# Performance work log

Measured on AMD Instinct MI355X. Metric: run time of the kernel, lower is better.

Reference implementation:

```python
import jax, jax.numpy as jnp
import numpy as np

NUM_HEADS = 16
HEAD_DIM = 32  # dim=512 / num_heads=16


def _rel_pos_bias(table, index, window_area):
    # table: [(2W-1)^2, H], index: [N, N] int -> bias [1, H, N, N]
    bias = table[index.reshape(-1)].reshape(window_area, window_area, -1)
    return jnp.transpose(bias, (2, 0, 1))[None]


def setup_inputs() -> dict:
    key = jax.random.key(0)
    ks = jax.random.split(key, 6)
    B, N, C = 256, 196, 512
    x = jax.random.normal(ks[0], (B, N, C), dtype=jnp.float32)
    qkv_w = jax.random.normal(ks[1], (3 * C, C), dtype=jnp.float32) * 0.02
    proj_w = jax.random.normal(ks[2], (C, C), dtype=jnp.float32) * 0.02
    proj_b = jax.random.normal(ks[3], (C,), dtype=jnp.float32) * 0.02
    rel_pos_bias_table = jax.random.normal(ks[4], (729, NUM_HEADS), dtype=jnp.float32) * 0.02
    rel_pos_index = jax.random.randint(ks[5], (N, N), 0, 729, dtype=jnp.int64)
    return {
        "x": x,
        "qkv_w": qkv_w,
        "proj_w": proj_w,
        "proj_b": proj_b,
        "rel_pos_bias_table": rel_pos_bias_table,
        "rel_pos_index": rel_pos_index,
        "window_area": N,
    }


def reference(x, qkv_w, proj_w, proj_b, rel_pos_bias_table, rel_pos_index, window_area):
    B, N, C = x.shape
    H, hd = NUM_HEADS, HEAD_DIM
    scale = hd ** -0.5
    # qkv projection (no bias), split into q,k,v: [B, H, N, hd]
    qkv = (x @ qkv_w.T).reshape(B, N, 3, H, hd)
    qkv = jnp.transpose(qkv, (2, 0, 3, 1, 4))
    q, k, v = qkv[0], qkv[1], qkv[2]
    attn = jnp.einsum("bhnd,bhmd->bhnm", q * scale, k)
    attn = attn + _rel_pos_bias(rel_pos_bias_table, rel_pos_index, window_area)
    attn = jax.nn.softmax(attn, axis=-1)
    out = jnp.einsum("bhnm,bhmd->bhnd", attn, v)
    out = jnp.transpose(out, (0, 2, 1, 3)).reshape(B, N, C)
    return out @ proj_w.T + proj_b
```

## Files before the change

kernel.cpp:

```cpp
#include <hip/hip_runtime.h>
#include <hip/hip_bf16.h>


typedef unsigned short u16;
typedef unsigned int u32;
typedef __attribute__((ext_vector_type(8))) short bf16x8;
typedef __attribute__((ext_vector_type(4))) float f32x4;

__device__ __forceinline__ u16 f2bf(float f) {
  union { float f; unsigned u; } c; c.f = f;
  unsigned r = ((c.u >> 16) & 1u) + 0x7fffu;
  return (u16)((c.u + r) >> 16);
}

__global__ __launch_bounds__(256) void cvt_f32_bf16(const float* __restrict__ in,
                                                    u16* __restrict__ out, int n) {
  int i = (blockIdx.x * 256 + threadIdx.x) * 4;
  if (i >= n) return;
  float4 v = *(const float4*)(in + i);
  ushort4 o;
  o.x = f2bf(v.x); o.y = f2bf(v.y); o.z = f2bf(v.z); o.w = f2bf(v.w);
  *(ushort4*)(out + i) = o;
}

__global__ __launch_bounds__(256) void zero_vt_pad(u16* __restrict__ vt) {
  int i = blockIdx.x * 256 + threadIdx.x;
  if (i >= 4096 * 32 * 36) return;
  int row = i / 36, c = i - row * 36;
  vt[row * 232 + 196 + c] = 0;
}

__global__ __launch_bounds__(256) void build_bias(const float* __restrict__ table,
                                                  const int* __restrict__ idx,
                                                  float* __restrict__ outb) {
  int e = blockIdx.x * 256 + threadIdx.x;
  int r = e & 3, lane = (e >> 2) & 63, rest = e >> 8;
  int mt = rest % 14; rest /= 14;
  int nt = rest % 13; int h = rest / 13;
  int n = nt * 16 + (lane & 15);
  int m = mt * 16 + ((lane >> 4) << 2) + r;
  float v;
  if (m < 196) {
    int nc = n < 196 ? n : 195;
    v = table[idx[nc * 196 + m] * 16 + h];
  } else {
    v = -1e30f;
  }
  outb[e] = v;
}

template<int EPI>
__global__ __launch_bounds__(512, 2) void gemm256(
    const u16* __restrict__ A, const u16* __restrict__ Bt,
    u16* __restrict__ q, u16* __restrict__ kk, u16* __restrict__ vt,
    const float* __restrict__ pbias, float* __restrict__ out) {
  constexpr int K = 512;
  constexpr int NWGX = (EPI == 0) ? 6 : 2;
  constexpr int NWG = NWGX * 196;
  __shared__ u16 LA[4][8192];
  __shared__ u16 LB[4][8192];

  int id = blockIdx.y * NWGX + blockIdx.x;
  int nf = (id & 7) * (NWG >> 3) + (id >> 3);
  const int bx = nf / NWGX, by = nf - (nf / NWGX) * NWGX;

  const int tid = threadIdx.x;
  const int w = tid >> 6, l = tid & 63;
  const int lr = l & 15, lg = l >> 4;
  const int wm = w >> 2, wn = w & 3;

  const int gq = (l & 3) ^ ((l >> 3) & 3);
  const u16* gA = A + (long)(bx * 256 + w * 32 + (l >> 2)) * K + gq * 8;
  const u16* gB = Bt + (long)(by * 256 + w * 32 + (l >> 2)) * K + gq * 8;

  const int swz = (lg ^ ((lr >> 1) & 3)) * 8;
  const int ra = (wm * 128 + lr) * 32 + swz;
  const int rb = (wn * 64 + lr) * 32 + swz;

#define STAGE_A(st, kt)                                                        \
  __builtin_amdgcn_global_load_lds((const __attribute__((address_space(1))) void*)(gA + (kt) * 32), \
      (__attribute__((address_space(3))) void*)&LA[st][w * 1024], 16, 0, 0);   \
  __builtin_amdgcn_global_load_lds((const __attribute__((address_space(1))) void*)(gA + 16 * K + (kt) * 32), \
      (__attribute__((address_space(3))) void*)&LA[st][w * 1024 + 512], 16, 0, 0);
#define STAGE_B(st, kt)                                                        \
  __builtin_amdgcn_global_load_lds((const __attribute__((address_space(1))) void*)(gB + (kt) * 32), \
      (__attribute__((address_space(3))) void*)&LB[st][w * 1024], 16, 0, 0);   \
  __builtin_amdgcn_global_load_lds((const __attribute__((address_space(1))) void*)(gB + 16 * K + (kt) * 32), \
      (__attribute__((address_space(3))) void*)&LB[st][w * 1024 + 512], 16, 0, 0);

  f32x4 acc[8][4] = {};
  bf16x8 bfr[4];

  STAGE_A(0, 0); STAGE_B(0, 0);
  STAGE_A(1, 1); STAGE_B(1, 1);
  STAGE_A(2, 2); STAGE_B(2, 2);
  asm volatile("s_waitcnt vmcnt(8)" ::: "memory");
  __builtin_amdgcn_s_barrier();

  for (int kt = 0; kt < 16; ++kt) {
    const int slot = kt & 3;
    const int st = (kt + 3) & 3;
    const int sk = (kt + 3 < 16) ? kt + 3 : 15;
    const u16* as = &LA[slot][0];
    const u16* bs = &LB[slot][0];

    bf16x8 afr[4];
#pragma unroll
    for (int f = 0; f < 4; ++f) afr[f] = *(const bf16x8*)&as[ra + f * 512];
#pragma unroll
    for (int j2 = 0; j2 < 4; ++j2) bfr[j2] = *(const bf16x8*)&bs[rb + j2 * 512];
    STAGE_A(st, sk);
    asm volatile("s_waitcnt vmcnt(8)" ::: "memory");
    __builtin_amdgcn_s_barrier();
    asm volatile("s_waitcnt lgkmcnt(0)" ::: "memory");
    __builtin_amdgcn_s_setprio(1);
#pragma unroll
    for (int f = 0; f < 4; ++f)
#pragma unroll
      for (int j2 = 0; j2 < 4; ++j2)
        acc[f][j2] = __builtin_amdgcn_mfma_f32_16x16x32_bf16(afr[f], bfr[j2], acc[f][j2], 0, 0, 0);
    __builtin_amdgcn_s_setprio(0);
    __builtin_amdgcn_s_barrier();

#pragma unroll
    for (int f = 0; f < 4; ++f) afr[f] = *(const bf16x8*)&as[ra + (f + 4) * 512];
    STAGE_B(st, sk);
    asm volatile("s_waitcnt vmcnt(8)" ::: "memory");
    __builtin_amdgcn_s_barrier();
    asm volatile("s_waitcnt lgkmcnt(0)" ::: "memory");
    __builtin_amdgcn_s_setprio(1);
#pragma unroll
    for (int f = 0; f < 4; ++f)
#pragma unroll
      for (int j2 = 0; j2 < 4; ++j2)
        acc[f + 4][j2] = __builtin_amdgcn_mfma_f32_16x16x32_bf16(afr[f], bfr[j2], acc[f + 4][j2], 0, 0, 0);
    __builtin_amdgcn_s_setprio(0);
    __builtin_amdgcn_s_barrier();
  }
#undef STAGE_A
#undef STAGE_B
  asm volatile("s_waitcnt vmcnt(0)" ::: "memory");

  const int colbase = by * 256 + wn * 64;
  const int rowb = bx * 256 + wm * 128 + lg * 4;
#pragma unroll
  for (int f = 0; f < 8; ++f) {
    const int row0 = rowb + f * 16;
    const int bb = row0 / 196;
    const int nn0 = row0 - bb * 196;
#pragma unroll
    for (int j2 = 0; j2 < 4; ++j2) {
      const int col = colbase + j2 * 16 + lr;
      if (EPI == 0) {
        const int t = col >> 9, h = (col >> 5) & 15, dd = col & 31;
        const long bh = (long)bb * 16 + h;
        if (t == 0) {
          const float s = 0.17677669529663687f;
#pragma unroll
          for (int r = 0; r < 4; ++r)
            q[(bh * 196 + nn0 + r) * 32 + dd] = f2bf(acc[f][j2][r] * s);
        } else if (t == 1) {
#pragma unroll
          for (int r = 0; r < 4; ++r)
            kk[(bh * 196 + nn0 + r) * 32 + dd] = f2bf(acc[f][j2][r]);
        } else {
          ushort4 pv;
          pv.x = f2bf(acc[f][j2][0]); pv.y = f2bf(acc[f][j2][1]);
          pv.z = f2bf(acc[f][j2][2]); pv.w = f2bf(acc[f][j2][3]);
          *(ushort4*)&vt[(bh * 32 + dd) * 232 + nn0] = pv;
        }
      } else {
        const float pb = pbias[col];
#pragma unroll
        for (int r = 0; r < 4; ++r)
          out[(long)(row0 + r) * 512 + col] = acc[f][j2][r] + pb;
      }
    }
  }
}

__global__ __launch_bounds__(256, 4) void attn_kernel(
    const u16* __restrict__ q, const u16* __restrict__ kk,
    const u16* __restrict__ vt, const float* __restrict__ biasA,
    u16* __restrict__ ao) {
  __shared__ u16 Ks[196 * 40];
  __shared__ u16 Vs[32 * 232];
  const int bhd = blockIdx.x;
  const int h = bhd >> 8, bb = bhd & 255;
  const int bh = bb * 16 + h;
  const int tid = threadIdx.x, w = tid >> 6, l = tid & 63;
  const int lr = l & 15, lg = l >> 4;

  {
    const u16* kg = kk + (long)bh * (196 * 32);
#pragma unroll
    for (int p = 0; p < 4; ++p) {
      int m = p * 64 + (tid >> 2);
      if (m < 196) {
        int c = (tid & 3) * 8;
        *(bf16x8*)&Ks[m * 40 + c] = *(const bf16x8*)(kg + m * 32 + c);
      }
    }
    const u16* vg = vt + (long)bh * (32 * 232);
#pragma unroll
    for (int p = 0; p < 4; ++p) {
      int off = (p * 256 + tid) * 8;
      if (off < 32 * 232) *(bf16x8*)&Vs[off] = *(const bf16x8*)(vg + off);
    }
  }
  __syncthreads();

  const float* biasH = biasA + (long)h * (13 * 14 * 256);
  const int sA = ((l & 16) << 1) + lr;
  const int sB = sA + 16;
  const bool hi = (l & 32) != 0;

  for (int nt = w; nt < 13; nt += 4) {
    int nq = nt * 16 + lr; if (nq > 195) nq = 195;
    bf16x8 qa = *(const bf16x8*)(q + ((long)bh * 196 + nq) * 32 + lg * 8);

    u32 pk[14][2];
    float ssum = 0.f;
#pragma unroll
    for (int mt = 0; mt < 14; ++mt) {
      int row = mt * 16 + lr; if (row > 195) row = 195;
      bf16x8 kb = *(const bf16x8*)&Ks[row * 40 + lg * 8];
      const float4 b4 = *(const float4*)(biasH + ((nt * 14 + mt) * 64 + l) * 4);
      f32x4 c; c[0] = b4.x; c[1] = b4.y; c[2] = b4.z; c[3] = b4.w;
      f32x4 S = __builtin_amdgcn_mfma_f32_16x16x32_bf16(kb, qa, c, 0, 0, 0);
      float e0 = __expf(S[0]), e1 = __expf(S[1]);
      float e2 = __expf(S[2]), e3 = __expf(S[3]);
      ssum += (e0 + e1) + (e2 + e3);
      asm("v_cvt_pk_bf16_f32 %0, %1, %2" : "=v"(pk[mt][0]) : "v"(e0), "v"(e1));
      asm("v_cvt_pk_bf16_f32 %0, %1, %2" : "=v"(pk[mt][1]) : "v"(e2), "v"(e3));
    }
    ssum += __shfl_xor(ssum, 16);
    ssum += __shfl_xor(ssum, 32);
    float invT = __builtin_amdgcn_rcpf(ssum);

    f32x4 O0 = {}, O1 = {};
#pragma unroll
    for (int ks = 0; ks < 7; ++ks) {
      u32 a0 = (u32)__shfl((int)pk[2 * ks][0], sA);
      u32 a1 = (u32)__shfl((int)pk[2 * ks][1], sA);
      u32 a2 = (u32)__shfl((int)pk[2 * ks][0], sB);
      u32 a3 = (u32)__shfl((int)pk[2 * ks][1], sB);
      u32 c0 = (u32)__shfl((int)pk[2 * ks + 1][0], sA);
      u32 c1 = (u32)__shfl((int)pk[2 * ks + 1][1], sA);
      u32 c2 = (u32)__shfl((int)pk[2 * ks + 1][0], sB);
      u32 c3 = (u32)__shfl((int)pk[2 * ks + 1][1], sB);
      bf16x8 pa;
      ((u32*)&pa)[0] = hi ? c0 : a0;
      ((u32*)&pa)[1] = hi ? c1 : a1;
      ((u32*)&pa)[2] = hi ? c2 : a2;
      ((u32*)&pa)[3] = hi ? c3 : a3;
      bf16x8 v0 = *(const bf16x8*)&Vs[lr * 232 + ks * 32 + lg * 8];
      bf16x8 v1 = *(const bf16x8*)&Vs[(16 + lr) * 232 + ks * 32 + lg * 8];
      O0 = __builtin_amdgcn_mfma_f32_16x16x32_bf16(pa, v0, O0, 0, 0, 0);
      O1 = __builtin_amdgcn_mfma_f32_16x16x32_bf16(pa, v1, O1, 0, 0, 0);
    }

    float inv[4];
#pragma unroll
    for (int r = 0; r < 4; ++r) inv[r] = __shfl(invT, lg * 4 + r);
    const int nr0 = nt * 16 + lg * 4;
#pragma unroll
    for (int r = 0; r < 4; ++r) {
      int nr = nr0 + r;
      if (nr < 196) {
        long base = ((long)bb * 196 + nr) * 512 + h * 32;
        ao[base + lr] = f2bf(O0[r] * inv[r]);
        ao[base + 16 + lr] = f2bf(O1[r] * inv[r]);
      }
    }
  }
}

extern "C" void kernel_launch(void* const* d_in, const int* in_sizes, int n_in,
                              void* d_out, int out_size, void* d_ws, size_t ws_size,
                              hipStream_t stream) {
  const float* x      = (const float*)d_in[0];
  const float* qkv_w  = (const float*)d_in[1];
  const float* proj_w = (const float*)d_in[2];
  const float* proj_b = (const float*)d_in[3];
  const float* table  = (const float*)d_in[4];
  const int*   ridx   = (const int*)d_in[5];
  float* out = (float*)d_out;

  char* ws = (char*)d_ws;
  u16*   xb    = (u16*)(ws);
  u16*   qwb   = (u16*)(ws + 51380224);
  u16*   pwb   = (u16*)(ws + 52953088);
  u16*   qb    = (u16*)(ws + 53477376);
  u16*   kb    = (u16*)(ws + 104857600);
  u16*   vtb   = (u16*)(ws + 156237824);
  float* biasA = (float*)(ws + 217055232);

  cvt_f32_bf16<<<25088, 256, 0, stream>>>(x, xb, 25690112);
  cvt_f32_bf16<<<768, 256, 0, stream>>>(qkv_w, qwb, 786432);
  cvt_f32_bf16<<<256, 256, 0, stream>>>(proj_w, pwb, 262144);
  build_bias<<<2912, 256, 0, stream>>>(table, ridx, biasA);
  zero_vt_pad<<<18432, 256, 0, stream>>>(vtb);

  gemm256<0><<<dim3(6, 196), 512, 0, stream>>>(xb, qwb, qb, kb, vtb, nullptr, nullptr);
  attn_kernel<<<4096, 256, 0, stream>>>(qb, kb, vtb, biasA, xb );
  gemm256<1><<<dim3(2, 196), 512, 0, stream>>>(xb, pwb, nullptr, nullptr, nullptr, proj_b, out);
}
```

Baseline: 295.9 us.

## Stage QKV epilogue through LDS, merge GEMM k-step phases, store bias as bf16

The QKV GEMM epilogue now writes the accumulator tile to shared memory (transposed for V) and then issues coalesced 16-byte stores to q, k and vt, replacing scattered 2-byte stores. The two half-step MFMA phases per k-tile are merged into one phase that loads all 8 A fragments at once, which removes a barrier pair per iteration but raises register pressure. The relative-position bias is stored in bf16 and widened in the attention kernel, halving its memory traffic at a small precision cost.

```diff
diff --git a/kernel.cpp b/kernel.cpp
--- a/kernel.cpp
+++ b/kernel.cpp
@@ -32,7 +32,7 @@
 
 __global__ __launch_bounds__(256) void build_bias(const float* __restrict__ table,
                                                   const int* __restrict__ idx,
-                                                  float* __restrict__ outb) {
+                                                  u16* __restrict__ outb) {
   int e = blockIdx.x * 256 + threadIdx.x;
   int r = e & 3, lane = (e >> 2) & 63, rest = e >> 8;
   int mt = rest % 14; rest /= 14;
@@ -46,7 +46,7 @@
   } else {
     v = -1e30f;
   }
-  outb[e] = v;
+  outb[e] = f2bf(v);
 }
 
 template<int EPI>
@@ -57,8 +57,9 @@
   constexpr int K = 512;
   constexpr int NWGX = (EPI == 0) ? 6 : 2;
   constexpr int NWG = NWGX * 196;
-  __shared__ u16 LA[4][8192];
-  __shared__ u16 LB[4][8192];
+  __shared__ __align__(16) u16 SMEM[65536];
+  u16* LA = SMEM;
+  u16* LB = SMEM + 32768;
 
   int id = blockIdx.y * NWGX + blockIdx.x;
   int nf = (id & 7) * (NWG >> 3) + (id >> 3);
@@ -79,17 +80,16 @@
 
 #define STAGE_A(st, kt)                                                        \
   __builtin_amdgcn_global_load_lds((const __attribute__((address_space(1))) void*)(gA + (kt) * 32), \
-      (__attribute__((address_space(3))) void*)&LA[st][w * 1024], 16, 0, 0);   \
+      (__attribute__((address_space(3))) void*)&LA[(st) * 8192 + w * 1024], 16, 0, 0); \
   __builtin_amdgcn_global_load_lds((const __attribute__((address_space(1))) void*)(gA + 16 * K + (kt) * 32), \
-      (__attribute__((address_space(3))) void*)&LA[st][w * 1024 + 512], 16, 0, 0);
+      (__attribute__((address_space(3))) void*)&LA[(st) * 8192 + w * 1024 + 512], 16, 0, 0);
 #define STAGE_B(st, kt)                                                        \
   __builtin_amdgcn_global_load_lds((const __attribute__((address_space(1))) void*)(gB + (kt) * 32), \
-      (__attribute__((address_space(3))) void*)&LB[st][w * 1024], 16, 0, 0);   \
+      (__attribute__((address_space(3))) void*)&LB[(st) * 8192 + w * 1024], 16, 0, 0); \
   __builtin_amdgcn_global_load_lds((const __attribute__((address_space(1))) void*)(gB + 16 * K + (kt) * 32), \
-      (__attribute__((address_space(3))) void*)&LB[st][w * 1024 + 512], 16, 0, 0);
+      (__attribute__((address_space(3))) void*)&LB[(st) * 8192 + w * 1024 + 512], 16, 0, 0);
 
   f32x4 acc[8][4] = {};
-  bf16x8 bfr[4];
 
   STAGE_A(0, 0); STAGE_B(0, 0);
   STAGE_A(1, 1); STAGE_B(1, 1);
@@ -101,39 +101,25 @@
     const int slot = kt & 3;
     const int st = (kt + 3) & 3;
     const int sk = (kt + 3 < 16) ? kt + 3 : 15;
-    const u16* as = &LA[slot][0];
-    const u16* bs = &LB[slot][0];
-
-    bf16x8 afr[4];
-#pragma unroll
-    for (int f = 0; f < 4; ++f) afr[f] = *(const bf16x8*)&as[ra + f * 512];
+    const u16* as = &LA[slot * 8192];
+    const u16* bs = &LB[slot * 8192];
+
+    bf16x8 afr[8], bfr[4];
+#pragma unroll
+    for (int f = 0; f < 8; ++f) afr[f] = *(const bf16x8*)&as[ra + f * 512];
 #pragma unroll
     for (int j2 = 0; j2 < 4; ++j2) bfr[j2] = *(const bf16x8*)&bs[rb + j2 * 512];
     STAGE_A(st, sk);
-    asm volatile("s_waitcnt vmcnt(8)" ::: "memory");
-    __builtin_amdgcn_s_barrier();
-    asm volatile("s_waitcnt lgkmcnt(0)" ::: "memory");
-    __builtin_amdgcn_s_setprio(1);
-#pragma unroll
-    for (int f = 0; f < 4; ++f)
-#pragma unroll
-      for (int j2 = 0; j2 < 4; ++j2)
-        acc[f][j2] = __builtin_amdgcn_mfma_f32_16x16x32_bf16(afr[f], bfr[j2], acc[f][j2], 0, 0, 0);
-    __builtin_amdgcn_s_setprio(0);
-    __builtin_amdgcn_s_barrier();
-
-#pragma unroll
-    for (int f = 0; f < 4; ++f) afr[f] = *(const bf16x8*)&as[ra + (f + 4) * 512];
     STAGE_B(st, sk);
     asm volatile("s_waitcnt vmcnt(8)" ::: "memory");
     __builtin_amdgcn_s_barrier();
     asm volatile("s_waitcnt lgkmcnt(0)" ::: "memory");
     __builtin_amdgcn_s_setprio(1);
 #pragma unroll
-    for (int f = 0; f < 4; ++f)
+    for (int f = 0; f < 8; ++f)
 #pragma unroll
       for (int j2 = 0; j2 < 4; ++j2)
-        acc[f + 4][j2] = __builtin_amdgcn_mfma_f32_16x16x32_bf16(afr[f], bfr[j2], acc[f + 4][j2], 0, 0, 0);
+        acc[f][j2] = __builtin_amdgcn_mfma_f32_16x16x32_bf16(afr[f], bfr[j2], acc[f][j2], 0, 0, 0);
     __builtin_amdgcn_s_setprio(0);
     __builtin_amdgcn_s_barrier();
   }
@@ -141,35 +127,80 @@
 #undef STAGE_B
   asm volatile("s_waitcnt vmcnt(0)" ::: "memory");
 
-  const int colbase = by * 256 + wn * 64;
-  const int rowb = bx * 256 + wm * 128 + lg * 4;
-#pragma unroll
-  for (int f = 0; f < 8; ++f) {
-    const int row0 = rowb + f * 16;
-    const int bb = row0 / 196;
-    const int nn0 = row0 - bb * 196;
-#pragma unroll
-    for (int j2 = 0; j2 < 4; ++j2) {
-      const int col = colbase + j2 * 16 + lr;
-      if (EPI == 0) {
-        const int t = col >> 9, h = (col >> 5) & 15, dd = col & 31;
-        const long bh = (long)bb * 16 + h;
-        if (t == 0) {
-          const float s = 0.17677669529663687f;
-#pragma unroll
-          for (int r = 0; r < 4; ++r)
-            q[(bh * 196 + nn0 + r) * 32 + dd] = f2bf(acc[f][j2][r] * s);
-        } else if (t == 1) {
-#pragma unroll
-          for (int r = 0; r < 4; ++r)
-            kk[(bh * 196 + nn0 + r) * 32 + dd] = f2bf(acc[f][j2][r]);
+  if (EPI == 0) {
+    const int t = by >> 1;
+    const int colbase = by * 256;
+    const float s = (t == 0) ? 0.17677669529663687f : 1.0f;
+#pragma unroll
+    for (int p = 0; p < 2; ++p) {
+      __syncthreads();
+      if (wm == p) {
+        if (t < 2) {
+#pragma unroll
+          for (int f = 0; f < 8; ++f)
+#pragma unroll
+            for (int j2 = 0; j2 < 4; ++j2)
+#pragma unroll
+              for (int r = 0; r < 4; ++r)
+                SMEM[(f * 16 + lg * 4 + r) * 264 + wn * 64 + j2 * 16 + lr] =
+                    f2bf(acc[f][j2][r] * s);
         } else {
-          ushort4 pv;
-          pv.x = f2bf(acc[f][j2][0]); pv.y = f2bf(acc[f][j2][1]);
-          pv.z = f2bf(acc[f][j2][2]); pv.w = f2bf(acc[f][j2][3]);
-          *(ushort4*)&vt[(bh * 32 + dd) * 232 + nn0] = pv;
+#pragma unroll
+          for (int f = 0; f < 8; ++f)
+#pragma unroll
+            for (int j2 = 0; j2 < 4; ++j2)
+#pragma unroll
+              for (int r = 0; r < 4; ++r)
+                SMEM[(wn * 64 + j2 * 16 + lr) * 136 + f * 16 + lg * 4 + r] =
+                    f2bf(acc[f][j2][r]);
+        }
+      }
+      __syncthreads();
+      const int growbase = bx * 256 + p * 128;
+      if (t < 2) {
+        u16* dst = (t == 0) ? q : kk;
+        const int lrow = tid >> 2, ch = tid & 3;
+        const int grow = growbase + lrow;
+        const int bb2 = grow / 196, nn = grow - bb2 * 196;
+#pragma unroll
+        for (int i = 0; i < 8; ++i) {
+          const int colle = (ch + i * 4) * 8;
+          bf16x8 vv = *(const bf16x8*)&SMEM[lrow * 264 + colle];
+          const int col = colbase + colle;
+          const int h = (col >> 5) & 15, dd = col & 31;
+          *(bf16x8*)&dst[((long)(bb2 * 16 + h) * 196 + nn) * 32 + dd] = vv;
         }
       } else {
+        const int cl = tid >> 1, half = tid & 1;
+        const int col = colbase + cl;
+        const int h = (col >> 5) & 15, dd = col & 31;
+#pragma unroll
+        for (int i = 0; i < 8; ++i) {
+          const int r0 = growbase + half * 64 + i * 8;
+          bf16x8 vv = *(const bf16x8*)&SMEM[cl * 136 + half * 64 + i * 8];
+          const int bb2 = r0 / 196, nn = r0 - bb2 * 196;
+          if (nn + 8 <= 196) {
+            *(bf16x8*)&vt[((long)(bb2 * 16 + h) * 32 + dd) * 232 + nn] = vv;
+          } else {
+#pragma unroll
+            for (int e = 0; e < 8; ++e) {
+              const int rr = r0 + e;
+              const int b3 = rr / 196, n3 = rr - b3 * 196;
+              vt[((long)(b3 * 16 + h) * 32 + dd) * 232 + n3] = (u16)((short*)&vv)[e];
+            }
+          }
+        }
+      }
+    }
+  } else {
+    const int colbase = by * 256 + wn * 64;
+    const int rowb = bx * 256 + wm * 128 + lg * 4;
+#pragma unroll
+    for (int f = 0; f < 8; ++f) {
+      const int row0 = rowb + f * 16;
+#pragma unroll
+      for (int j2 = 0; j2 < 4; ++j2) {
+        const int col = colbase + j2 * 16 + lr;
         const float pb = pbias[col];
 #pragma unroll
         for (int r = 0; r < 4; ++r)
@@ -181,7 +212,7 @@
 
 __global__ __launch_bounds__(256, 4) void attn_kernel(
     const u16* __restrict__ q, const u16* __restrict__ kk,
-    const u16* __restrict__ vt, const float* __restrict__ biasA,
+    const u16* __restrict__ vt, const u16* __restrict__ biasA,
     u16* __restrict__ ao) {
   __shared__ u16 Ks[196 * 40];
   __shared__ u16 Vs[32 * 232];
@@ -210,7 +241,7 @@
   }
   __syncthreads();
 
-  const float* biasH = biasA + (long)h * (13 * 14 * 256);
+  const u16* biasH = biasA + (long)h * (13 * 14 * 256);
   const int sA = ((l & 16) << 1) + lr;
   const int sB = sA + 16;
   const bool hi = (l & 32) != 0;
@@ -225,8 +256,12 @@
     for (int mt = 0; mt < 14; ++mt) {
       int row = mt * 16 + lr; if (row > 195) row = 195;
       bf16x8 kb = *(const bf16x8*)&Ks[row * 40 + lg * 8];
-      const float4 b4 = *(const float4*)(biasH + ((nt * 14 + mt) * 64 + l) * 4);
-      f32x4 c; c[0] = b4.x; c[1] = b4.y; c[2] = b4.z; c[3] = b4.w;
+      const ushort4 b4 = *(const ushort4*)(biasH + ((nt * 14 + mt) * 64 + l) * 4);
+      f32x4 c;
+      c[0] = __uint_as_float(((u32)b4.x) << 16);
+      c[1] = __uint_as_float(((u32)b4.y) << 16);
+      c[2] = __uint_as_float(((u32)b4.z) << 16);
+      c[3] = __uint_as_float(((u32)b4.w) << 16);
       f32x4 S = __builtin_amdgcn_mfma_f32_16x16x32_bf16(kb, qa, c, 0, 0, 0);
       float e0 = __expf(S[0]), e1 = __expf(S[1]);
       float e2 = __expf(S[2]), e3 = __expf(S[3]);
@@ -294,7 +329,7 @@
   u16*   qb    = (u16*)(ws + 53477376);
   u16*   kb    = (u16*)(ws + 104857600);
   u16*   vtb   = (u16*)(ws + 156237824);
-  float* biasA = (float*)(ws + 217055232);
+  u16*   biasA = (u16*)(ws + 217055232);
 
   cvt_f32_bf16<<<25088, 256, 0, stream>>>(x, xb, 25690112);
   cvt_f32_bf16<<<768, 256, 0, stream>>>(qkv_w, qwb, 786432);
```

After: 280.5 us. 1.06x faster.
